# Performance work log

Measured on AMD Instinct MI355X. Metric: run time of the kernel, lower is better.

## Reference

```python
import jax, jax.numpy as jnp
import numpy as np

EPS = 1e-12  # torch F.normalize eps
RBF_SCALE = 10.0


def _l2norm(x, axis=-1):
    n = jnp.sqrt(jnp.sum(x * x, axis=axis, keepdims=True))
    return x / jnp.maximum(n, EPS)


def setup_inputs() -> dict:
    key = jax.random.key(0)
    k1, k2, k3 = jax.random.split(key, 3)
    N, D, C = 32768, 1024, 2048
    inp = jax.random.normal(k1, (N, D), dtype=jnp.float32)
    pos = jax.random.normal(k2, (C, D), dtype=jnp.float32)
    # offset is initialized to zeros in torch; use small random values so the
    # output is non-trivial for kernel correctness testing.
    offset = 0.01 * jax.random.normal(k3, (C, D), dtype=jnp.float32)
    return {"inp": inp, "pos": pos, "offset": offset}


def reference(inp, pos, offset):
    a = _l2norm(inp)                       # [N, D]
    b = _l2norm(pos)                       # [C, D]
    dist = 1.0 - jnp.einsum('nd,cd->nc', a, b)   # [N, C] cosine distance
    w = jnp.exp(-RBF_SCALE * dist)               # RBF cluster weights
    # The torch for-loop  out += offset[i] * dist[:, i, None]  is a GEMM:
    out = inp + jnp.einsum('nc,cd->nd', w, offset)
    out = _l2norm(out)
    offset_reg = jnp.sum(offset * offset)
    return (out, offset_reg)
```

## Files before the change

kernel.cpp:

```cpp
#include <hip/hip_runtime.h>

typedef float  f32x4  __attribute__((ext_vector_type(4)));
typedef float  f32x16 __attribute__((ext_vector_type(16)));
typedef int    i32x4  __attribute__((ext_vector_type(4)));
typedef int    i32x8  __attribute__((ext_vector_type(8)));

#define AS1 __attribute__((address_space(1)))
#define AS3 __attribute__((address_space(3)))

__device__ __forceinline__ unsigned int f2e4m3(float x){
    union{float f; unsigned u;} v; v.f = x;
    unsigned s = (v.u >> 24) & 0x80u;
    float ax = fabsf(x);
    if (ax > 448.0f) ax = 448.0f;
    if (ax < 0.015625f){
        int d = (int)__builtin_rintf(ax * 512.0f);
        return s | (unsigned)d;
    }
    v.f = ax;
    unsigned u = v.u + 0x7ffffu + ((v.u >> 20) & 1u);
    unsigned E = (u >> 23) - 120u;
    unsigned M = (u >> 20) & 7u;
    return s | (E << 3) | M;
}

__device__ __forceinline__ unsigned int pk4(float x0, float x1, float x2, float x3){
#if __has_builtin(__builtin_amdgcn_cvt_pk_fp8_f32)
    int u = __builtin_amdgcn_cvt_pk_fp8_f32(x0, x1, 0, false);
    u     = __builtin_amdgcn_cvt_pk_fp8_f32(x2, x3, u, true);
    return (unsigned)u;
#else
    return f2e4m3(x0) | (f2e4m3(x1) << 8) | (f2e4m3(x2) << 16) | (f2e4m3(x3) << 24);
#endif
}

__device__ __forceinline__ void gload16(const unsigned char* g, const char* l){
    __builtin_amdgcn_global_load_lds((const AS1 void*)g, (AS3 void*)l, 16, 0, 0);
}

__device__ __forceinline__ i32x8 ld_frag(const char* p0, const char* p1){
    i32x4 lo = *(const i32x4*)p0;
    i32x4 hi = *(const i32x4*)p1;
    return __builtin_shufflevector(lo, hi, 0,1,2,3,4,5,6,7);
}

#define GBAR() do{ asm volatile("" ::: "memory"); __builtin_amdgcn_s_barrier(); \
                   asm volatile("" ::: "memory"); }while(0)
#define VMW(N)  asm volatile("s_waitcnt vmcnt(" #N ")" ::: "memory")

__global__ __launch_bounds__(256) void norm_rows_fp8_rm(const float* __restrict__ in,
                                                        unsigned int* __restrict__ out){
    const int row = blockIdx.x;
    const int t   = threadIdx.x;
    f32x4 x = ((const f32x4*)(in + (size_t)row * 1024))[t];
    float ss = x[0]*x[0] + x[1]*x[1] + x[2]*x[2] + x[3]*x[3];
    #pragma unroll
    for (int o = 32; o > 0; o >>= 1) ss += __shfl_xor(ss, o);
    __shared__ float red[4];
    if ((t & 63) == 0) red[t >> 6] = ss;
    __syncthreads();
    float tot = red[0] + red[1] + red[2] + red[3];
    float inv = 16.0f / fmaxf(sqrtf(tot), 1e-12f);
    out[(size_t)row * 256 + t] = pk4(x[0]*inv, x[1]*inv, x[2]*inv, x[3]*inv);
}

__global__ __launch_bounds__(256) void norm_rows_fp8_fl(const float* __restrict__ in,
                                                        unsigned char* __restrict__ out){
    const int row = blockIdx.x;
    const int t   = threadIdx.x;
    f32x4 x = ((const f32x4*)(in + (size_t)row * 1024))[t];
    float ss = x[0]*x[0] + x[1]*x[1] + x[2]*x[2] + x[3]*x[3];
    #pragma unroll
    for (int o = 32; o > 0; o >>= 1) ss += __shfl_xor(ss, o);
    __shared__ float red[4];
    if ((t & 63) == 0) red[t >> 6] = ss;
    __syncthreads();
    float tot = red[0] + red[1] + red[2] + red[3];
    float inv = 16.0f / fmaxf(sqrtf(tot), 1e-12f);
    unsigned u = pk4(x[0]*inv, x[1]*inv, x[2]*inv, x[3]*inv);
    size_t addr = ((size_t)(row >> 5) * 16 + (t >> 4)) * 2048
                + (size_t)((t >> 3) & 1) * 1024
                + (size_t)(row & 31) * 32 + ((4 * t) & 31);
    *(unsigned int*)(out + addr) = u;
}

__global__ __launch_bounds__(256) void norm_rows_f32(float* __restrict__ buf){
    const int row = blockIdx.x;
    const int t   = threadIdx.x;
    f32x4* p = (f32x4*)(buf + (size_t)row * 1024);
    f32x4 x = p[t];
    float ss = x[0]*x[0] + x[1]*x[1] + x[2]*x[2] + x[3]*x[3];
    #pragma unroll
    for (int o = 32; o > 0; o >>= 1) ss += __shfl_xor(ss, o);
    __shared__ float red[4];
    if ((t & 63) == 0) red[t >> 6] = ss;
    __syncthreads();
    float tot = red[0] + red[1] + red[2] + red[3];
    float inv = 1.0f / fmaxf(sqrtf(tot), 1e-12f);
    p[t] = x * inv;
}

__global__ __launch_bounds__(256) void transpose_off(const float* __restrict__ off,
                                                     unsigned char* __restrict__ offt,
                                                     float* __restrict__ reg_out){
    __shared__ unsigned char t_lds[64][68];
    const int t  = threadIdx.x;
    const int c0 = blockIdx.x * 64;
    const int d0 = blockIdx.y * 64;
    float ss = 0.f;
    #pragma unroll
    for (int p = 0; p < 4; ++p){
        int c  = p * 16 + (t >> 4);
        int dq = t & 15;
        f32x4 v = *(const f32x4*)(off + (size_t)(c0 + c) * 1024 + d0 + dq * 4);
        ss += v[0]*v[0] + v[1]*v[1] + v[2]*v[2] + v[3]*v[3];
        unsigned u = pk4(v[0]*64.0f, v[1]*64.0f, v[2]*64.0f, v[3]*64.0f);
        #pragma unroll
        for (int j = 0; j < 4; ++j) t_lds[dq * 4 + j][c] = (unsigned char)(u >> (8*j));
    }
    __syncthreads();
    #pragma unroll
    for (int i = 0; i < 4; ++i){
        int byte_o = (t + 256 * i) * 4;
        int fs  = byte_o >> 11;
        int rem = byte_o & 2047;
        int dl  = fs * 32 + ((rem >> 5) & 31);
        int cl  = ((rem >> 10) & 1) * 32 + (rem & 31);
        unsigned int v = *(const unsigned int*)&t_lds[dl][cl];
        size_t f = (size_t)((d0 >> 5) + fs);
        *(unsigned int*)(offt + (f * 32 + (c0 >> 6)) * 2048 + rem) = v;
    }
    #pragma unroll
    for (int o = 32; o > 0; o >>= 1) ss += __shfl_xor(ss, o);
    __shared__ float red[4];
    if ((t & 63) == 0) red[t >> 6] = ss;
    __syncthreads();
    if (t == 0) atomicAdd(reg_out, red[0] + red[1] + red[2] + red[3]);
}

template<int EPI, int SA, int SB>
__global__ __launch_bounds__(512, 2)
void gemm_hyb(const unsigned char* __restrict__ A, int lda,
              const unsigned char* __restrict__ B,
              int K,
              unsigned char* __restrict__ Wout, int ldw,
              const float* __restrict__ Cadd, float* __restrict__ Fout, int ldo)
{
    extern __shared__ char smem[];
    const int tid = threadIdx.x;

    int bx = blockIdx.x, by = blockIdx.y;
    {
        const int gx = gridDim.x, gy = gridDim.y;
        const int nwg = gx * gy;
        if ((nwg & 7) == 0){
            const int lid = bx + gx * by;
            const int q   = nwg >> 3;
            const int n   = (lid & 7) * q + (lid >> 3);
            const int sh  = 31 - __clz(gy);
            bx = n >> sh;
            by = n & (gy - 1);
        }
    }
    const int m0  = bx * 256;
    const int n0  = by * 256;
    const int wid = tid >> 6, lane = tid & 63;
    const int wr  = wid >> 2, wc = wid & 3;
    const int l31 = lane & 31, hg = lane >> 5;
    const int NT  = K >> 6;

    const int srow = tid >> 2;
    const int sg   = (tid & 3) ^ ((tid >> 3) & 3);
    const unsigned char* sA = A + (size_t)(m0 + srow) * lda + sg * 16;
    const int lp = tid * 16;
    auto stgA = [&](int buf, int ke){
        char* wb = smem + buf * 16384;
        gload16(sA + ke, wb + lp);
        gload16(sA + (size_t)128 * lda + ke, wb + 8192 + lp);
    };

    int aoff[4][2];
    #pragma unroll
    for (int m = 0; m < 4; ++m){
        int row = wr * 128 + m * 32 + l31;
        int sw  = (row >> 1) & 3;
        aoff[m][0] = row * 64 + (((hg << 1) | 0) ^ sw) * 16;
        aoff[m][1] = row * 64 + (((hg << 1) | 1) ^ sw) * 16;
    }

    const char* pB[2];
    #pragma unroll
    for (int n = 0; n < 2; ++n)
        pB[n] = (const char*)B
              + (size_t)(((n0 + wc * 64 + n * 32) >> 5) * NT) * 2048 + lane * 32;

    f32x16 acc[4][2] = {};
    i32x8 fa[4], bcur[2], bnxt[2];

#define MFMA8(bv) { __builtin_amdgcn_s_setprio(1); \
    _Pragma("unroll") for (int mi = 0; mi < 4; ++mi) \
    _Pragma("unroll") for (int ni = 0; ni < 2; ++ni) \
        acc[mi][ni] = __builtin_amdgcn_mfma_scale_f32_32x32x64_f8f6f4( \
            fa[mi], bv[ni], acc[mi][ni], 0, 0, 0, SA, 0, SB); \
    __builtin_amdgcn_s_setprio(0); }

    stgA(0, 0);
    stgA(1, 64);
    #pragma unroll
    for (int n = 0; n < 2; ++n) bcur[n] = ld_frag(pB[n], pB[n] + 16);
    VMW(6);
    GBAR();

    int bufc = 0;
    #pragma unroll 1
    for (int t = 0; t < NT - 1; ++t){
        const char* rb = smem + bufc * 16384;
        #pragma unroll
        for (int m = 0; m < 4; ++m)
            fa[m] = ld_frag(rb + aoff[m][0], rb + aoff[m][1]);
        {
            const size_t o = (size_t)(t + 1) * 2048;
            #pragma unroll
            for (int n = 0; n < 2; ++n) bnxt[n] = ld_frag(pB[n] + o, pB[n] + o + 16);
        }
        MFMA8(bcur);
        VMW(4);
        GBAR();
        if (t + 2 < NT){
            int bs = bufc + 2; if (bs >= 3) bs -= 3;
            stgA(bs, (t + 2) * 64);
        }
        bcur[0] = bnxt[0]; bcur[1] = bnxt[1];
        ++bufc; if (bufc == 3) bufc = 0;
    }
    {
        const char* rb = smem + bufc * 16384;
        #pragma unroll
        for (int m = 0; m < 4; ++m)
            fa[m] = ld_frag(rb + aoff[m][0], rb + aoff[m][1]);
        MFMA8(bcur);
    }
#undef MFMA8

    asm volatile("s_nop 7\n\ts_nop 7");

    #pragma unroll
    for (int m = 0; m < 4; ++m){
        #pragma unroll
        for (int n = 0; n < 2; ++n){
            const int grb = m0 + wr * 128 + m * 32;
            const int gc  = n0 + wc * 64  + n * 32 + l31;
            if (EPI == 1){
                #pragma unroll
                for (int q = 0; q < 4; ++q){
                    const int row0 = grb + 8 * q + 4 * hg;
                    float w0 = exp2f(fmaf(14.4269504f, acc[m][n][4*q+0], -4.4269504f));
                    float w1 = exp2f(fmaf(14.4269504f, acc[m][n][4*q+1], -4.4269504f));
                    float w2 = exp2f(fmaf(14.4269504f, acc[m][n][4*q+2], -4.4269504f));
                    float w3 = exp2f(fmaf(14.4269504f, acc[m][n][4*q+3], -4.4269504f));
                    unsigned u = pk4(w0, w1, w2, w3);
                    unsigned char* p = Wout + (size_t)row0 * ldw + gc;
                    p[0]                = (unsigned char)u;
                    p[(size_t)ldw]      = (unsigned char)(u >> 8);
                    p[(size_t)ldw * 2]  = (unsigned char)(u >> 16);
                    p[(size_t)ldw * 3]  = (unsigned char)(u >> 24);
                }
            } else {
                #pragma unroll
                for (int r = 0; r < 16; ++r){
                    const int row = (r & 3) + 8 * (r >> 2) + 4 * hg;
                    Fout[(size_t)(grb + row) * ldo + gc] =
                        Cadd[(size_t)(grb + row) * ldo + gc] + acc[m][n][r];
                }
            }
        }
    }
}

extern "C" void kernel_launch(void* const* d_in, const int* in_sizes, int n_in,
                              void* d_out, int out_size, void* d_ws, size_t ws_size,
                              hipStream_t stream)
{
    (void)n_in; (void)out_size;
    const float* inp = (const float*)d_in[0];
    const float* pos = (const float*)d_in[1];
    const float* off = (const float*)d_in[2];
    float* out = (float*)d_out;

    const int D = 1024, C = 2048;
    const int N = in_sizes[0] / D;

    unsigned char* b_fp8 = (unsigned char*)d_ws;
    unsigned char* offt  = b_fp8 + (size_t)C * D;
    unsigned char* a_fp8 = offt + (size_t)D * C;
    size_t fixed = (size_t)C * D * 2;
    size_t avail = ws_size > fixed ? ws_size - fixed : 0;
    int Mc = 256;
    for (int cand = N; cand >= 256; cand >>= 1){
        if ((size_t)cand * (size_t)(D + C) <= avail){ Mc = cand; break; }
    }
    if (Mc > N) Mc = N;
    unsigned char* w_buf = a_fp8 + (size_t)Mc * D;

    hipFuncSetAttribute(reinterpret_cast<const void*>(&gemm_hyb<1,123,123>),
                        hipFuncAttributeMaxDynamicSharedMemorySize, 49152);
    hipFuncSetAttribute(reinterpret_cast<const void*>(&gemm_hyb<2,117,121>),
                        hipFuncAttributeMaxDynamicSharedMemorySize, 49152);

    float* reg_out = out + (size_t)N * D;
    hipMemsetAsync(reg_out, 0, sizeof(float), stream);

    transpose_off<<<dim3(C / 64, D / 64), 256, 0, stream>>>(off, offt, reg_out);
    norm_rows_fp8_fl<<<C, 256, 0, stream>>>(pos, b_fp8);

    for (int r0 = 0; r0 < N; r0 += Mc){
        norm_rows_fp8_rm<<<Mc, 256, 0, stream>>>(inp + (size_t)r0 * D, (unsigned int*)a_fp8);
        gemm_hyb<1,123,123><<<dim3(Mc / 256, C / 256), 512, 49152, stream>>>(
            a_fp8, D, b_fp8, D, w_buf, C, nullptr, nullptr, 0);
        gemm_hyb<2,117,121><<<dim3(Mc / 256, D / 256), 512, 49152, stream>>>(
            w_buf, C, offt, C, nullptr, 0, inp + (size_t)r0 * D, out + (size_t)r0 * D, D);
    }
    norm_rows_f32<<<N, 256, 0, stream>>>(out);
}
```

Measured before the change: 289.2 us.

## Fuse residual add and final row L2-normalize into second GEMM epilogue

Replaces the second GEMM plus separate normalization pass with a new kernel where each workgroup owns 64 full output rows across all 1024 columns. It adds the input residual, reduces per-row sum of squares via shuffles and LDS, then writes normalized output directly. This removes a full read-modify-write pass over the 128MB fp32 output. In exchange, tiles become 64x1024 with B fragments streamed straight from global memory, which changes data reuse and occupancy and may weaken the GEMM itself.

```diff
diff --git a/kernel.cpp b/kernel.cpp
--- a/kernel.cpp
+++ b/kernel.cpp
@@ -84,22 +84,6 @@
     *(unsigned int*)(out + addr) = u;
 }
 
-__global__ __launch_bounds__(256) void norm_rows_f32(float* __restrict__ buf){
-    const int row = blockIdx.x;
-    const int t   = threadIdx.x;
-    f32x4* p = (f32x4*)(buf + (size_t)row * 1024);
-    f32x4 x = p[t];
-    float ss = x[0]*x[0] + x[1]*x[1] + x[2]*x[2] + x[3]*x[3];
-    #pragma unroll
-    for (int o = 32; o > 0; o >>= 1) ss += __shfl_xor(ss, o);
-    __shared__ float red[4];
-    if ((t & 63) == 0) red[t >> 6] = ss;
-    __syncthreads();
-    float tot = red[0] + red[1] + red[2] + red[3];
-    float inv = 1.0f / fmaxf(sqrtf(tot), 1e-12f);
-    p[t] = x * inv;
-}
-
 __global__ __launch_bounds__(256) void transpose_off(const float* __restrict__ off,
                                                      unsigned char* __restrict__ offt,
                                                      float* __restrict__ reg_out){
@@ -148,7 +132,6 @@
 {
     extern __shared__ char smem[];
     const int tid = threadIdx.x;
-
     int bx = blockIdx.x, by = blockIdx.y;
     {
         const int gx = gridDim.x, gy = gridDim.y;
@@ -187,7 +170,6 @@
         aoff[m][0] = row * 64 + (((hg << 1) | 0) ^ sw) * 16;
         aoff[m][1] = row * 64 + (((hg << 1) | 1) ^ sw) * 16;
     }
-
     const char* pB[2];
     #pragma unroll
     for (int n = 0; n < 2; ++n)
@@ -277,6 +259,141 @@
     }
 }
 
+template<int SA, int SB>
+__global__ __launch_bounds__(512, 2)
+void gemm_norm(const unsigned char* __restrict__ W,
+               const unsigned char* __restrict__ Boff,
+               const float* __restrict__ inp,
+               float* __restrict__ out)
+{
+    extern __shared__ char smem[];
+    const int tid = threadIdx.x;
+    int b = blockIdx.x;
+    {
+        const int nwg = gridDim.x;
+        if ((nwg & 7) == 0){ const int q = nwg >> 3; b = (b & 7) * q + (b >> 3); }
+    }
+    const int r0  = b * 64;
+    const int wid = tid >> 6, lane = tid & 63;
+    const int wr  = wid >> 2, wc = wid & 3;
+    const int l31 = lane & 31, hg = lane >> 5;
+    const int NT  = 32;
+    const int NU  = 8;
+
+    const int s_row = tid >> 4;
+    const int s_col = ((tid & 15) ^ (s_row & 15)) * 16;
+    auto stgA = [&](int buf, int u){
+        char* wb = smem + buf * 16384;
+        const unsigned char* base = W + (size_t)u * 256 + s_col;
+        gload16(base + (size_t)(r0 + s_row)      * 2048, wb + tid * 16);
+        gload16(base + (size_t)(r0 + 32 + s_row) * 2048, wb + 8192 + tid * 16);
+    };
+
+    int aoff[4][2];
+    {
+        const int row = wr * 32 + l31;
+        const int sw  = row & 15;
+        #pragma unroll
+        for (int kk = 0; kk < 4; ++kk){
+            aoff[kk][0] = row * 256 + ((kk * 4 + hg * 2 + 0) ^ sw) * 16;
+            aoff[kk][1] = row * 256 + ((kk * 4 + hg * 2 + 1) ^ sw) * 16;
+        }
+    }
+
+    const char* pB[8];
+    #pragma unroll
+    for (int n = 0; n < 8; ++n)
+        pB[n] = (const char*)Boff + (size_t)(wc * 8 + n) * NT * 2048 + lane * 32;
+
+    f32x16 acc[8] = {};
+    i32x8 fa, b0[4], b1[4];
+
+    stgA(0, 0);
+    stgA(1, 1);
+    VMW(2);
+    #pragma unroll
+    for (int n = 0; n < 4; ++n) b0[n] = ld_frag(pB[n],     pB[n] + 16);
+    #pragma unroll
+    for (int n = 0; n < 4; ++n) b1[n] = ld_frag(pB[n + 4], pB[n + 4] + 16);
+    GBAR();
+
+    #pragma unroll 1
+    for (int u = 0; u < NU; ++u){
+        const char* rb = smem + (u % 3) * 16384;
+        #pragma unroll
+        for (int kk = 0; kk < 4; ++kk){
+            const int t = u * 4 + kk;
+            fa = ld_frag(rb + aoff[kk][0], rb + aoff[kk][1]);
+            const size_t on = (size_t)(t + 1 < NT ? t + 1 : NT - 1) * 2048;
+            __builtin_amdgcn_s_setprio(1);
+            #pragma unroll
+            for (int n = 0; n < 4; ++n)
+                acc[n] = __builtin_amdgcn_mfma_scale_f32_32x32x64_f8f6f4(
+                    fa, b0[n], acc[n], 0, 0, 0, SA, 0, SB);
+            __builtin_amdgcn_s_setprio(0);
+            #pragma unroll
+            for (int n = 0; n < 4; ++n) b0[n] = ld_frag(pB[n] + on, pB[n] + on + 16);
+            __builtin_amdgcn_s_setprio(1);
+            #pragma unroll
+            for (int n = 0; n < 4; ++n)
+                acc[n + 4] = __builtin_amdgcn_mfma_scale_f32_32x32x64_f8f6f4(
+                    fa, b1[n], acc[n + 4], 0, 0, 0, SA, 0, SB);
+            __builtin_amdgcn_s_setprio(0);
+            #pragma unroll
+            for (int n = 0; n < 4; ++n) b1[n] = ld_frag(pB[n+4] + on, pB[n+4] + on + 16);
+        }
+        if (u + 1 < NU) VMW(16);
+        GBAR();
+        if (u + 2 < NU) stgA((u + 2) % 3, u + 2);
+    }
+
+    asm volatile("s_nop 7\n\ts_nop 7");
+
+    float ss[16];
+    #pragma unroll
+    for (int r = 0; r < 16; ++r) ss[r] = 0.f;
+    const int grow0 = r0 + wr * 32;
+    #pragma unroll
+    for (int n = 0; n < 8; ++n){
+        const int col = wc * 256 + n * 32 + l31;
+        #pragma unroll
+        for (int r = 0; r < 16; ++r){
+            const int row = (r & 3) + 8 * (r >> 2) + 4 * hg;
+            float vv = inp[(size_t)(grow0 + row) * 1024 + col] + acc[n][r];
+            acc[n][r] = vv;
+            ss[r] += vv * vv;
+        }
+    }
+    #pragma unroll
+    for (int m = 1; m <= 16; m <<= 1)
+        #pragma unroll
+        for (int r = 0; r < 16; ++r) ss[r] += __shfl_xor(ss[r], m);
+
+    float* ssb = (float*)smem;
+    GBAR();
+    if (l31 == 0){
+        #pragma unroll
+        for (int r = 0; r < 16; ++r){
+            const int row = (r & 3) + 8 * (r >> 2) + 4 * hg;
+            ssb[(wr * 32 + row) * 4 + wc] = ss[r];
+        }
+    }
+    GBAR();
+    #pragma unroll
+    for (int r = 0; r < 16; ++r){
+        const int row = (r & 3) + 8 * (r >> 2) + 4 * hg;
+        const float* q = &ssb[(wr * 32 + row) * 4];
+        float tot = q[0] + q[1] + q[2] + q[3];
+        float inv = 1.0f / fmaxf(sqrtf(tot), 1e-12f);
+        const size_t rbase = (size_t)(grow0 + row) * 1024;
+        #pragma unroll
+        for (int n = 0; n < 8; ++n){
+            const int col = wc * 256 + n * 32 + l31;
+            out[rbase + col] = acc[n][r] * inv;
+        }
+    }
+}
+
 extern "C" void kernel_launch(void* const* d_in, const int* in_sizes, int n_in,
                               void* d_out, int out_size, void* d_ws, size_t ws_size,
                               hipStream_t stream)
@@ -304,7 +421,7 @@
 
     hipFuncSetAttribute(reinterpret_cast<const void*>(&gemm_hyb<1,123,123>),
                         hipFuncAttributeMaxDynamicSharedMemorySize, 49152);
-    hipFuncSetAttribute(reinterpret_cast<const void*>(&gemm_hyb<2,117,121>),
+    hipFuncSetAttribute(reinterpret_cast<const void*>(&gemm_norm<117,121>),
                         hipFuncAttributeMaxDynamicSharedMemorySize, 49152);
 
     float* reg_out = out + (size_t)N * D;
@@ -317,8 +434,7 @@
         norm_rows_fp8_rm<<<Mc, 256, 0, stream>>>(inp + (size_t)r0 * D, (unsigned int*)a_fp8);
         gemm_hyb<1,123,123><<<dim3(Mc / 256, C / 256), 512, 49152, stream>>>(
             a_fp8, D, b_fp8, D, w_buf, C, nullptr, nullptr, 0);
-        gemm_hyb<2,117,121><<<dim3(Mc / 256, D / 256), 512, 49152, stream>>>(
-            w_buf, C, offt, C, nullptr, 0, inp + (size_t)r0 * D, out + (size_t)r0 * D, D);
-    }
-    norm_rows_f32<<<N, 256, 0, stream>>>(out);
-}
+        gemm_norm<117,121><<<Mc / 64, 512, 49152, stream>>>(
+            w_buf, offt, inp + (size_t)r0 * D, out + (size_t)r0 * D);
+    }
+}
```

Measured after the change: 1.007 ms. 248% more time.
